# Kernel tuning notes

Hardware: AMD Instinct MI355X
Metric: run time of the kernel (lower is better)

The kernel has to match this reference:

```python
import jax
jax.config.update("jax_enable_x64", True)
import jax.numpy as jnp
import numpy as np

N_QUBITS = 12
DIM = 2 ** N_QUBITS  # 4096
M = 4096             # number of state-vector columns
TWO_PI = 2.0 * np.pi


def _u3(t):
    """Single-qubit U3 gate (2x2 complex128) from 3 Euler angles, matching the TF code."""
    t = t.astype(jnp.complex128)
    c = jnp.cos(t[0] / 2)
    s = jnp.sin(t[0] / 2)
    row0 = jnp.stack([c, -jnp.exp(1j * t[2]) * s])
    row1 = jnp.stack([jnp.exp(1j * t[1]) * s, jnp.exp(1j * (t[1] + t[2])) * c])
    return jnp.stack([row0, row1])  # [2, 2] complex128


def setup_inputs() -> dict:
    key = jax.random.key(0)
    k1, k2, k3 = jax.random.split(key, 3)
    thetas = jax.random.uniform(k1, (N_QUBITS, 3), dtype=jnp.float64,
                                minval=0.0, maxval=TWO_PI)
    inputs_re = jax.random.normal(k2, (DIM, M), dtype=jnp.float64)
    inputs_im = jax.random.normal(k3, (DIM, M), dtype=jnp.float64)
    return {"thetas": thetas, "inputs_re": inputs_re, "inputs_im": inputs_im}


def reference(thetas, inputs_re, inputs_im):
    # Build full 2^n x 2^n unitary as Kronecker product of per-qubit U3 gates
    # (same association order as the recursive tensor() in the TF code:
    #  U3(q0) (x) U3(q1) (x) ... (x) U3(q_{n-1})).
    gates = [_u3(thetas[i]) for i in range(N_QUBITS)]  # small fixed loop
    U = gates[0]
    for g in gates[1:]:
        U = jnp.kron(U, g)  # [DIM, DIM] complex128
    x = inputs_re.astype(jnp.complex128) + 1j * inputs_im.astype(jnp.complex128)
    return U @ x  # [DIM, M] complex128
```

## Files before the change

### kernel.cpp

```cpp
#include <hip/hip_runtime.h>

#define MCOL 4096

__device__ __forceinline__ float rfl(float x) {
    return __int_as_float(__builtin_amdgcn_readfirstlane(__float_as_int(x)));
}

__device__ __forceinline__ unsigned f2bf(float f) {
    unsigned u = __float_as_uint(f);
    u += 0x7fffu + ((u >> 16) & 1u);
    return u >> 16;
}

__device__ __forceinline__ bool looks_like_thetas(const float* p) {
    bool ok = true;
    #pragma unroll
    for (int i = 0; i < 36; ++i) {
        float v = p[i];
        ok = ok && (v >= 0.0f) && (v <= 6.2831855f);
    }
    return ok;
}

__device__ __forceinline__ unsigned g4c(const uint4& v, int c) {
    return c == 0 ? v.x : c == 1 ? v.y : c == 2 ? v.z : v.w;
}
__device__ __forceinline__ void s4c(uint4& v, int c, unsigned x) {
    if (c == 0) v.x = x; else if (c == 1) v.y = x; else if (c == 2) v.z = x; else v.w = x;
}

struct Gates {
    float ar[6];
    float br[6], bi[6];
    float cr[6], ci[6];
    float dr[6], di[6];
};

template <int QBASE>
__device__ __forceinline__ void compute_gates(const float* __restrict__ thetas, Gates& g) {
    #pragma unroll
    for (int b = 0; b < 6; ++b) {
        const int q = QBASE - b;
        float t0 = thetas[3 * q + 0];
        float t1 = thetas[3 * q + 1];
        float t2 = thetas[3 * q + 2];
        float ch = cosf(0.5f * t0), sh = sinf(0.5f * t0);
        float c1 = cosf(t1), s1 = sinf(t1);
        float c2 = cosf(t2), s2 = sinf(t2);
        float c12 = cosf(t1 + t2), s12 = sinf(t1 + t2);
        g.ar[b] = rfl(ch);
        g.br[b] = rfl(-c2 * sh);  g.bi[b] = rfl(-s2 * sh);
        g.cr[b] = rfl(c1 * sh);   g.ci[b] = rfl(s1 * sh);
        g.dr[b] = rfl(c12 * ch);  g.di[b] = rfl(s12 * ch);
    }
}

struct Gates3 {
    float ar[3];
    float br[3], bi[3];
    float cr[3], ci[3];
    float dr[3], di[3];
};

template <int QBASE>
__device__ __forceinline__ void compute_gates3(const float* __restrict__ thetas, Gates3& g) {
    #pragma unroll
    for (int b = 0; b < 3; ++b) {
        const int q = QBASE - b;
        float t0 = thetas[3 * q + 0];
        float t1 = thetas[3 * q + 1];
        float t2 = thetas[3 * q + 2];
        float ch = cosf(0.5f * t0), sh = sinf(0.5f * t0);
        float c1 = cosf(t1), s1 = sinf(t1);
        float c2 = cosf(t2), s2 = sinf(t2);
        float c12 = cosf(t1 + t2), s12 = sinf(t1 + t2);
        g.ar[b] = rfl(ch);
        g.br[b] = rfl(-c2 * sh);  g.bi[b] = rfl(-s2 * sh);
        g.cr[b] = rfl(c1 * sh);   g.ci[b] = rfl(s1 * sh);
        g.dr[b] = rfl(c12 * ch);  g.di[b] = rfl(s12 * ch);
    }
}

__device__ __forceinline__ void butterflies(float (&vr)[64], float (&vi)[64], const Gates& g) {
    #pragma unroll
    for (int b = 0; b < 6; ++b) {
        const int s = 1 << b;
        #pragma unroll
        for (int l = 0; l < 64; ++l) {
            if ((l & s) == 0) {
                const int m = l | s;
                float x0r = vr[l], x0i = vi[l];
                float x1r = vr[m], x1i = vi[m];
                float n0r = g.ar[b] * x0r + g.br[b] * x1r - g.bi[b] * x1i;
                float n0i = g.ar[b] * x0i + g.br[b] * x1i + g.bi[b] * x1r;
                float n1r = g.cr[b] * x0r - g.ci[b] * x0i + g.dr[b] * x1r - g.di[b] * x1i;
                float n1i = g.cr[b] * x0i + g.ci[b] * x0r + g.dr[b] * x1i + g.di[b] * x1r;
                vr[l] = n0r; vi[l] = n0i;
                vr[m] = n1r; vi[m] = n1i;
            }
        }
    }
}

__device__ __forceinline__ void butterflies8(float (&vr)[8], float (&vi)[8], const Gates3& g) {
    #pragma unroll
    for (int b = 0; b < 3; ++b) {
        const int s = 1 << b;
        #pragma unroll
        for (int k = 0; k < 8; ++k) {
            if ((k & s) == 0) {
                const int m = k | s;
                float x0r = vr[k], x0i = vi[k];
                float x1r = vr[m], x1i = vi[m];
                float n0r = g.ar[b] * x0r + g.br[b] * x1r - g.bi[b] * x1i;
                float n0i = g.ar[b] * x0i + g.br[b] * x1i + g.bi[b] * x1r;
                float n1r = g.cr[b] * x0r - g.ci[b] * x0i + g.dr[b] * x1r - g.di[b] * x1i;
                float n1i = g.cr[b] * x0i + g.ci[b] * x0r + g.dr[b] * x1i + g.di[b] * x1r;
                vr[k] = n0r; vi[k] = n0i;
                vr[m] = n1r; vi[m] = n1i;
            }
        }
    }
}

__global__ __launch_bounds__(256, 1) void k_low(const float* __restrict__ p0,
                                                const float* __restrict__ p1,
                                                const float* __restrict__ p2,
                                                unsigned int* __restrict__ out) {
    const bool dictorder = looks_like_thetas(p0);
    const float* thetas = dictorder ? p0 : p2;
    const float* xre    = p1;
    const float* xim    = dictorder ? p2 : p0;

    Gates g;
    compute_gates<11>(thetas, g);
    const int t = threadIdx.x;
    const int lane = t & 63, wave = t >> 6;
    const int h  = blockIdx.x & 63;
    const int jb = blockIdx.x >> 6;
    const int j  = (jb << 8) + (wave << 6) + lane;
    const int base = (h << 6) * MCOL + j;

    float vr[64], vi[64];
    #pragma unroll
    for (int l = 0; l < 64; ++l) {
        vr[l] = xre[base + l * MCOL];
        vi[l] = xim[base + l * MCOL];
    }

    butterflies(vr, vi, g);

    if (dictorder) {
        #pragma unroll
        for (int l = 0; l < 64; ++l)
            out[base + l * MCOL] = f2bf(vi[l]) | (f2bf(vr[l]) << 16);
    } else {
        #pragma unroll
        for (int l = 0; l < 64; ++l)
            out[base + l * MCOL] = f2bf(vr[l]) | (f2bf(vi[l]) << 16);
    }
}

__global__ __launch_bounds__(256) void k_high(const float* __restrict__ p0,
                                              const float* __restrict__ p2,
                                              unsigned int* __restrict__ io) {
    const bool dictorder = looks_like_thetas(p0);
    const float* thetas = dictorder ? p0 : p2;

    Gates3 g;
    compute_gates3<5>(thetas, g);
    const int t = threadIdx.x;
    const int lhb = blockIdx.x & 511;
    const int l  = lhb & 63;
    const int hb = lhb >> 6;
    const int cg = blockIdx.x >> 9;
    const int jcol = (cg << 10) + (t << 2);
    const int base = ((hb << 9) + l) * MCOL + jcol;

    uint4 pk[8];
    #pragma unroll
    for (int ha = 0; ha < 8; ++ha)
        pk[ha] = *reinterpret_cast<const uint4*>(&io[base + (ha << 6) * MCOL]);

    uint4 res[8];
    #pragma unroll
    for (int c = 0; c < 4; ++c) {
        float vr[8], vi[8];
        #pragma unroll
        for (int ha = 0; ha < 8; ++ha) {
            const unsigned w = g4c(pk[ha], c);
            if (dictorder) {
                vi[ha] = __uint_as_float(w << 16);
                vr[ha] = __uint_as_float(w & 0xffff0000u);
            } else {
                vr[ha] = __uint_as_float(w << 16);
                vi[ha] = __uint_as_float(w & 0xffff0000u);
            }
        }
        butterflies8(vr, vi, g);
        #pragma unroll
        for (int ha = 0; ha < 8; ++ha) {
            const unsigned w = dictorder ? (f2bf(vi[ha]) | (f2bf(vr[ha]) << 16))
                                         : (f2bf(vr[ha]) | (f2bf(vi[ha]) << 16));
            s4c(res[ha], c, w);
        }
    }

    #pragma unroll
    for (int ha = 0; ha < 8; ++ha)
        *reinterpret_cast<uint4*>(&io[base + (ha << 6) * MCOL]) = res[ha];
}

__global__ __launch_bounds__(256) void k_high2(const float* __restrict__ p0,
                                               const float* __restrict__ p2,
                                               unsigned int* __restrict__ io) {
    const bool dictorder = looks_like_thetas(p0);
    const float* thetas = dictorder ? p0 : p2;

    Gates3 g;
    compute_gates3<2>(thetas, g);
    const int t = threadIdx.x;
    const int lha = blockIdx.x & 511;
    const int l  = lha & 63;
    const int ha = lha >> 6;
    const int cg = blockIdx.x >> 9;
    const int jcol = (cg << 10) + (t << 2);
    const int base = ((ha << 6) + l) * MCOL + jcol;

    uint4 pk[8];
    #pragma unroll
    for (int hb = 0; hb < 8; ++hb)
        pk[hb] = *reinterpret_cast<const uint4*>(&io[base + (hb << 9) * MCOL]);

    uint4 res[8];
    #pragma unroll
    for (int c = 0; c < 4; ++c) {
        float vr[8], vi[8];
        #pragma unroll
        for (int hb = 0; hb < 8; ++hb) {
            const unsigned w = g4c(pk[hb], c);
            if (dictorder) {
                vi[hb] = __uint_as_float(w << 16);
                vr[hb] = __uint_as_float(w & 0xffff0000u);
            } else {
                vr[hb] = __uint_as_float(w << 16);
                vi[hb] = __uint_as_float(w & 0xffff0000u);
            }
        }
        butterflies8(vr, vi, g);
        #pragma unroll
        for (int hb = 0; hb < 8; ++hb) {
            const unsigned w = dictorder ? (f2bf(vi[hb]) | (f2bf(vr[hb]) << 16))
                                         : (f2bf(vr[hb]) | (f2bf(vi[hb]) << 16));
            s4c(res[hb], c, w);
        }
    }

    #pragma unroll
    for (int hb = 0; hb < 8; ++hb)
        *reinterpret_cast<uint4*>(&io[base + (hb << 9) * MCOL]) = res[hb];
}

extern "C" void kernel_launch(void* const* d_in, const int* in_sizes, int n_in,
                              void* d_out, int out_size, void* d_ws, size_t ws_size,
                              hipStream_t stream) {
    const float* p0 = (const float*)d_in[0];
    const float* p1 = (const float*)d_in[1];
    const float* p2 = (const float*)d_in[2];
    unsigned int* out = (unsigned int*)d_out;

    dim3 block(256);
    dim3 grid(64 * 16);
    dim3 gridH(512 * 4);

    hipLaunchKernelGGL(k_low,   grid,  block, 0, stream, p0, p1, p2, out);
    hipLaunchKernelGGL(k_high,  gridH, block, 0, stream, p0, p2, out);
    hipLaunchKernelGGL(k_high2, gridH, block, 0, stream, p0, p2, out);
}
```

Before: 130.9 us.

## Split six-qubit low pass into two vectorized three-qubit passes

Replaces the single low-qubit kernel, which held 64 complex rows per thread in registers at one block per CU, with two kernels that each apply three qubits. Each new kernel uses float4/uint4 loads and stores of 8 rows by 4 columns per thread. The aim is far lower register pressure, higher occupancy and wider memory accesses. The cost is an extra full read-modify-write pass over the bf16-packed intermediate, which adds an extra launch and more global memory traffic.

```diff
diff --git a/kernel.cpp b/kernel.cpp
--- a/kernel.cpp
+++ b/kernel.cpp
@@ -28,31 +28,8 @@
 __device__ __forceinline__ void s4c(uint4& v, int c, unsigned x) {
     if (c == 0) v.x = x; else if (c == 1) v.y = x; else if (c == 2) v.z = x; else v.w = x;
 }
-
-struct Gates {
-    float ar[6];
-    float br[6], bi[6];
-    float cr[6], ci[6];
-    float dr[6], di[6];
-};
-
-template <int QBASE>
-__device__ __forceinline__ void compute_gates(const float* __restrict__ thetas, Gates& g) {
-    #pragma unroll
-    for (int b = 0; b < 6; ++b) {
-        const int q = QBASE - b;
-        float t0 = thetas[3 * q + 0];
-        float t1 = thetas[3 * q + 1];
-        float t2 = thetas[3 * q + 2];
-        float ch = cosf(0.5f * t0), sh = sinf(0.5f * t0);
-        float c1 = cosf(t1), s1 = sinf(t1);
-        float c2 = cosf(t2), s2 = sinf(t2);
-        float c12 = cosf(t1 + t2), s12 = sinf(t1 + t2);
-        g.ar[b] = rfl(ch);
-        g.br[b] = rfl(-c2 * sh);  g.bi[b] = rfl(-s2 * sh);
-        g.cr[b] = rfl(c1 * sh);   g.ci[b] = rfl(s1 * sh);
-        g.dr[b] = rfl(c12 * ch);  g.di[b] = rfl(s12 * ch);
-    }
+__device__ __forceinline__ float g4f(const float4& v, int c) {
+    return c == 0 ? v.x : c == 1 ? v.y : c == 2 ? v.z : v.w;
 }
 
 struct Gates3 {
@@ -81,27 +58,6 @@
     }
 }
 
-__device__ __forceinline__ void butterflies(float (&vr)[64], float (&vi)[64], const Gates& g) {
-    #pragma unroll
-    for (int b = 0; b < 6; ++b) {
-        const int s = 1 << b;
-        #pragma unroll
-        for (int l = 0; l < 64; ++l) {
-            if ((l & s) == 0) {
-                const int m = l | s;
-                float x0r = vr[l], x0i = vi[l];
-                float x1r = vr[m], x1i = vi[m];
-                float n0r = g.ar[b] * x0r + g.br[b] * x1r - g.bi[b] * x1i;
-                float n0i = g.ar[b] * x0i + g.br[b] * x1i + g.bi[b] * x1r;
-                float n1r = g.cr[b] * x0r - g.ci[b] * x0i + g.dr[b] * x1r - g.di[b] * x1i;
-                float n1i = g.cr[b] * x0i + g.ci[b] * x0r + g.dr[b] * x1i + g.di[b] * x1r;
-                vr[l] = n0r; vi[l] = n0i;
-                vr[m] = n1r; vi[m] = n1i;
-            }
-        }
-    }
-}
-
 __device__ __forceinline__ void butterflies8(float (&vr)[8], float (&vi)[8], const Gates3& g) {
     #pragma unroll
     for (int b = 0; b < 3; ++b) {
@@ -123,42 +79,102 @@
     }
 }
 
-__global__ __launch_bounds__(256, 1) void k_low(const float* __restrict__ p0,
-                                                const float* __restrict__ p1,
-                                                const float* __restrict__ p2,
-                                                unsigned int* __restrict__ out) {
+
+__global__ __launch_bounds__(256) void k_lowA(const float* __restrict__ p0,
+                                              const float* __restrict__ p1,
+                                              const float* __restrict__ p2,
+                                              unsigned int* __restrict__ out) {
     const bool dictorder = looks_like_thetas(p0);
     const float* thetas = dictorder ? p0 : p2;
     const float* xre    = p1;
     const float* xim    = dictorder ? p2 : p0;
 
-    Gates g;
-    compute_gates<11>(thetas, g);
-    const int t = threadIdx.x;
-    const int lane = t & 63, wave = t >> 6;
-    const int h  = blockIdx.x & 63;
-    const int jb = blockIdx.x >> 6;
-    const int j  = (jb << 8) + (wave << 6) + lane;
-    const int base = (h << 6) * MCOL + j;
-
-    float vr[64], vi[64];
-    #pragma unroll
-    for (int l = 0; l < 64; ++l) {
-        vr[l] = xre[base + l * MCOL];
-        vi[l] = xim[base + l * MCOL];
-    }
-
-    butterflies(vr, vi, g);
-
-    if (dictorder) {
-        #pragma unroll
-        for (int l = 0; l < 64; ++l)
-            out[base + l * MCOL] = f2bf(vi[l]) | (f2bf(vr[l]) << 16);
-    } else {
-        #pragma unroll
-        for (int l = 0; l < 64; ++l)
-            out[base + l * MCOL] = f2bf(vr[l]) | (f2bf(vi[l]) << 16);
-    }
+    Gates3 g;
+    compute_gates3<11>(thetas, g);
+    const int t = threadIdx.x;
+    const int rg = blockIdx.x & 511;
+    const int cg = blockIdx.x >> 9;
+    const int jcol = (cg << 10) + (t << 2);
+    const int base = (rg << 3) * MCOL + jcol;
+
+    float4 re[8], im[8];
+    #pragma unroll
+    for (int k = 0; k < 8; ++k) {
+        re[k] = *reinterpret_cast<const float4*>(&xre[base + k * MCOL]);
+        im[k] = *reinterpret_cast<const float4*>(&xim[base + k * MCOL]);
+    }
+
+    uint4 res[8];
+    #pragma unroll
+    for (int c = 0; c < 4; ++c) {
+        float vr[8], vi[8];
+        #pragma unroll
+        for (int k = 0; k < 8; ++k) {
+            vr[k] = g4f(re[k], c);
+            vi[k] = g4f(im[k], c);
+        }
+        butterflies8(vr, vi, g);
+        #pragma unroll
+        for (int k = 0; k < 8; ++k) {
+            const unsigned w = dictorder ? (f2bf(vi[k]) | (f2bf(vr[k]) << 16))
+                                         : (f2bf(vr[k]) | (f2bf(vi[k]) << 16));
+            s4c(res[k], c, w);
+        }
+    }
+
+    #pragma unroll
+    for (int k = 0; k < 8; ++k)
+        *reinterpret_cast<uint4*>(&out[base + k * MCOL]) = res[k];
+}
+
+__global__ __launch_bounds__(256) void k_lowB(const float* __restrict__ p0,
+                                              const float* __restrict__ p2,
+                                              unsigned int* __restrict__ io) {
+    const bool dictorder = looks_like_thetas(p0);
+    const float* thetas = dictorder ? p0 : p2;
+
+    Gates3 g;
+    compute_gates3<8>(thetas, g);
+    const int t = threadIdx.x;
+    const int rg = blockIdx.x & 511;
+    const int lo3 = rg & 7;
+    const int hi6 = rg >> 3;
+    const int cg = blockIdx.x >> 9;
+    const int jcol = (cg << 10) + (t << 2);
+    const int base = ((hi6 << 6) + lo3) * MCOL + jcol;
+
+    uint4 pk[8];
+    #pragma unroll
+    for (int k = 0; k < 8; ++k)
+        pk[k] = *reinterpret_cast<const uint4*>(&io[base + (k << 3) * MCOL]);
+
+    uint4 res[8];
+    #pragma unroll
+    for (int c = 0; c < 4; ++c) {
+        float vr[8], vi[8];
+        #pragma unroll
+        for (int k = 0; k < 8; ++k) {
+            const unsigned w = g4c(pk[k], c);
+            if (dictorder) {
+                vi[k] = __uint_as_float(w << 16);
+                vr[k] = __uint_as_float(w & 0xffff0000u);
+            } else {
+                vr[k] = __uint_as_float(w << 16);
+                vi[k] = __uint_as_float(w & 0xffff0000u);
+            }
+        }
+        butterflies8(vr, vi, g);
+        #pragma unroll
+        for (int k = 0; k < 8; ++k) {
+            const unsigned w = dictorder ? (f2bf(vi[k]) | (f2bf(vr[k]) << 16))
+                                         : (f2bf(vr[k]) | (f2bf(vi[k]) << 16));
+            s4c(res[k], c, w);
+        }
+    }
+
+    #pragma unroll
+    for (int k = 0; k < 8; ++k)
+        *reinterpret_cast<uint4*>(&io[base + (k << 3) * MCOL]) = res[k];
 }
 
 __global__ __launch_bounds__(256) void k_high(const float* __restrict__ p0,
@@ -270,10 +286,10 @@
     unsigned int* out = (unsigned int*)d_out;
 
     dim3 block(256);
-    dim3 grid(64 * 16);
     dim3 gridH(512 * 4);
 
-    hipLaunchKernelGGL(k_low,   grid,  block, 0, stream, p0, p1, p2, out);
+    hipLaunchKernelGGL(k_lowA,  gridH, block, 0, stream, p0, p1, p2, out);
+    hipLaunchKernelGGL(k_lowB,  gridH, block, 0, stream, p0, p2, out);
     hipLaunchKernelGGL(k_high,  gridH, block, 0, stream, p0, p2, out);
     hipLaunchKernelGGL(k_high2, gridH, block, 0, stream, p0, p2, out);
 }
```

New measurement: 143.2 us. 1.09x slower.
